# Optimization experiments

Measured on AMD Instinct MI355X. Metric: run time of the kernel, lower is better.

## Reference

```python
import jax, jax.numpy as jnp
import numpy as np

B, DIM, H, W = 8, 384, 64, 64
HEADS, KD, RATIO = 8, 32, 2
D = RATIO * KD            # 64, per-head value dim
NH_KD = HEADS * KD        # 256
DH = HEADS * D            # 512
N = H * W


def conv1x1_bn(x, Wc, scale, bias):
    # 1x1 conv (no bias) + BatchNorm2d in eval mode folds to per-channel affine.
    y = jnp.einsum('bchw,oc->bohw', x, Wc)
    return y * scale[:, None, None] + bias[:, None, None]


def setup_inputs() -> dict:
    key = jax.random.key(0)
    ks = jax.random.split(key, 13)
    f32 = jnp.float32
    inp = {
        'x': jax.random.normal(ks[0], (B, DIM, H, W), f32),
        'Wq': jax.random.normal(ks[1], (NH_KD, DIM), f32) * (1.0 / np.sqrt(DIM)),
        'sq': jax.random.uniform(ks[2], (NH_KD,), f32, 0.5, 1.5),
        'bq': jax.random.normal(ks[3], (NH_KD,), f32) * 0.1,
        'Wk': jax.random.normal(ks[4], (NH_KD, DIM), f32) * (1.0 / np.sqrt(DIM)),
        'sk': jax.random.uniform(ks[5], (NH_KD,), f32, 0.5, 1.5),
        'bk': jax.random.normal(ks[6], (NH_KD,), f32) * 0.1,
        'Wv': jax.random.normal(ks[7], (DH, DIM), f32) * (1.0 / np.sqrt(DIM)),
        'sv': jax.random.uniform(ks[8], (DH,), f32, 0.5, 1.5),
        'bv': jax.random.normal(ks[9], (DH,), f32) * 0.1,
        'Wp': jax.random.normal(ks[10], (DIM, DH), f32) * (1.0 / np.sqrt(DH)),
        'sp': jax.random.uniform(ks[11], (DIM,), f32, 0.5, 1.5),
        'bp': jax.random.normal(ks[12], (DIM,), f32) * 0.1,
    }
    return inp


def reference(x, Wq, sq, bq, Wk, sk, bk, Wv, sv, bv, Wp, sp, bp):
    # Q/K/V projections (1x1 conv + BN), reshaped to per-head [B, h, c, N]
    q = conv1x1_bn(x, Wq, sq, bq).reshape(B, HEADS, KD, N)
    k = conv1x1_bn(x, Wk, sk, bk).reshape(B, HEADS, KD, N)
    v = conv1x1_bn(x, Wv, sv, bv).reshape(B, HEADS, D, N)
    # dual softmax: keys over spatial dim, queries over channel dim
    key_sm = jax.nn.softmax(k, axis=3)
    query_sm = jax.nn.softmax(q, axis=2)
    # context = key @ value^T : [B,h,kd,d]
    context = jnp.einsum('bhkn,bhdn->bhkd', key_sm, v)
    # attended = context^T @ query : [B,h,d,N]
    attended = jnp.einsum('bhkd,bhkn->bhdn', context, query_sm)
    attended = attended.reshape(B, DH, H, W)
    # proj: activation (ReLU) then 1x1 conv + BN
    out = conv1x1_bn(jax.nn.relu(attended), Wp, sp, bp)
    return out
```

## Files before the change

kernel.cpp:

```cpp
#include <hip/hip_runtime.h>

typedef __attribute__((ext_vector_type(8))) short bf16x8;
typedef __attribute__((ext_vector_type(4))) float f32x4;
typedef __attribute__((ext_vector_type(4))) unsigned short us4;

__device__ __forceinline__ unsigned short f2bf(float f) {
    unsigned int u = __builtin_bit_cast(unsigned int, f);
    u = (u + 0x7FFFu + ((u >> 16) & 1u)) >> 16;
    return (unsigned short)u;
}
__device__ __forceinline__ float bf2f(unsigned short h) {
    return __builtin_bit_cast(float, (unsigned int)h << 16);
}

__global__ __launch_bounds__(256) void fold_weights_k(
    const float* __restrict__ Wq, const float* __restrict__ sq, const float* __restrict__ bq,
    const float* __restrict__ Wk, const float* __restrict__ sk, const float* __restrict__ bk,
    const float* __restrict__ Wv, const float* __restrict__ sv, const float* __restrict__ bv,
    const float* __restrict__ Wp, const float* __restrict__ sp,
    unsigned short* __restrict__ WqkvP, unsigned short* __restrict__ Wpf, float* __restrict__ bqkvP)
{
    int i = blockIdx.x * 256 + threadIdx.x;
    if (i < 393216) {
        int r = i / 384, c = i - r * 384;
        int head = r >> 7, t = r & 127;
        float w, s;
        if (t < 32)      { int ch = head * 32 + t;        w = Wq[ch * 384 + c]; s = sq[ch]; }
        else if (t < 64) { int ch = head * 32 + (t - 32); w = Wk[ch * 384 + c]; s = sk[ch]; }
        else             { int ch = head * 64 + (t - 64); w = Wv[ch * 384 + c]; s = sv[ch]; }
        WqkvP[i] = f2bf(w * s);
    } else if (i < 589824) {
        int j = i - 393216;
        Wpf[j] = f2bf(Wp[j] * sp[j >> 9]);
    } else if (i < 590848) {
        int r = i - 589824;
        int head = r >> 7, t = r & 127;
        bqkvP[r] = (t < 32) ? bq[head * 32 + t]
                 : (t < 64) ? bk[head * 32 + (t - 32)]
                            : bv[head * 64 + (t - 64)];
    }
}

__global__ __launch_bounds__(256, 3) void gemm_qkv_k(
    const unsigned short* __restrict__ A,
    const float* __restrict__ x,
    const float* __restrict__ bias,
    unsigned short* __restrict__ q_out,
    float* __restrict__ part,
    float* __restrict__ psums)
{
    __shared__ unsigned short As[3 * 4096];
    __shared__ unsigned short Bs[3 * 4096];
    const int tid = threadIdx.x;
    const int lane = tid & 63;
    const int w = tid >> 6, wr = w >> 1, wc = w & 1;
    const int li = lane & 15, g = lane >> 4;
    const int b = blockIdx.z, head = blockIdx.y, chunk = blockIdx.x;
    const int n0 = chunk * 128, m0 = head * 128;
    const float* xb = x + (long)b * 384 * 4096 + n0 + 2 * lane;

    const int i0 = tid, i1 = tid + 256;
    const int p0 = i0 >> 3, v0 = (i0 & 7) ^ (p0 & 7);
    const int p1 = i1 >> 3, v1 = (i1 & 7) ^ (p1 & 7);
    const long aro0 = (long)m0 * 384 + (long)(p0 * 2 + (v0 >> 2)) * 384 + (v0 & 3) * 8;
    const long aro1 = (long)m0 * 384 + (long)(p1 * 2 + (v1 >> 2)) * 384 + (v1 & 3) * 8;

#define ISSUE_A(kt) { const int _bf = (kt) % 3; const int _k0 = (kt) * 32; \
    __builtin_amdgcn_global_load_lds( \
        (const __attribute__((address_space(1))) void*)(A + aro0 + _k0), \
        (__attribute__((address_space(3))) void*)(As + _bf * 4096 + (size_t)i0 * 8), 16, 0, 0); \
    __builtin_amdgcn_global_load_lds( \
        (const __attribute__((address_space(1))) void*)(A + aro1 + _k0), \
        (__attribute__((address_space(3))) void*)(As + _bf * 4096 + (size_t)i1 * 8), 16, 0, 0); }

#define ISSUE_B(kt, breg) { const int _k0 = (kt) * 32 + w * 8; \
    _Pragma("unroll") \
    for (int j = 0; j < 8; ++j) \
        breg[j] = *reinterpret_cast<const float2*>(xb + (long)(_k0 + j) * 4096); }

#define WRITE_B(breg, _bf) { \
    unsigned int pw0[4], pw1[4]; \
    _Pragma("unroll") \
    for (int j = 0; j < 4; ++j) { \
        asm("v_cvt_pk_bf16_f32 %0, %1, %2" : "=v"(pw0[j]) : "v"(breg[2*j].x), "v"(breg[2*j+1].x)); \
        asm("v_cvt_pk_bf16_f32 %0, %1, %2" : "=v"(pw1[j]) : "v"(breg[2*j].y), "v"(breg[2*j+1].y)); \
    } \
    uint4 q0 = {pw0[0], pw0[1], pw0[2], pw0[3]}; \
    uint4 q1 = {pw1[0], pw1[1], pw1[2], pw1[3]}; \
    int s0 = w ^ (lane & 7), s1 = (4 + w) ^ (lane & 7); \
    *reinterpret_cast<uint4*>(Bs + (_bf) * 4096 + lane * 64 + s0 * 8) = q0; \
    *reinterpret_cast<uint4*>(Bs + (_bf) * 4096 + lane * 64 + s1 * 8) = q1; }

    float2 bregA[8], bregB[8];
    ISSUE_A(0); ISSUE_B(0, bregA);
    ISSUE_A(1); ISSUE_B(1, bregB);
    WRITE_B(bregA, 0);
    asm volatile("s_waitcnt vmcnt(10) lgkmcnt(0)\n\ts_barrier" ::: "memory");
    __builtin_amdgcn_sched_barrier(0);

    f32x4 acc[4][4];
    #pragma unroll
    for (int i = 0; i < 4; ++i)
        #pragma unroll
        for (int j = 0; j < 4; ++j) acc[i][j] = (f32x4){0.f, 0.f, 0.f, 0.f};

    #pragma unroll
    for (int kt = 0; kt < 12; ++kt) {
        const unsigned short* Ab = As + (kt % 3) * 4096;
        const unsigned short* Bl = Bs + (kt % 3) * 4096;

        bf16x8 av[4], bv[4];
        #pragma unroll
        for (int mf = 0; mf < 4; ++mf) {
            int r = wr * 64 + mf * 16 + li;
            int p = r >> 1;
            int slot = (((r & 1) * 4 + g) ^ (p & 7));
            av[mf] = *reinterpret_cast<const bf16x8*>(Ab + p * 64 + slot * 8);
        }
        #pragma unroll
        for (int nf = 0; nf < 4; ++nf) {
            int r = wc * 64 + nf * 16 + li;
            int p = r >> 1;
            int slot = (((r & 1) * 4 + g) ^ (p & 7));
            bv[nf] = *reinterpret_cast<const bf16x8*>(Bl + p * 64 + slot * 8);
        }
        if (kt < 10) {
            ISSUE_A(kt + 2);
            if (kt & 1) { ISSUE_B(kt + 2, bregB) }
            else        { ISSUE_B(kt + 2, bregA) }
        }
        __builtin_amdgcn_s_setprio(1);
        #pragma unroll
        for (int mf = 0; mf < 4; ++mf)
            #pragma unroll
            for (int nf = 0; nf < 4; ++nf)
                acc[mf][nf] = __builtin_amdgcn_mfma_f32_16x16x32_bf16(av[mf], bv[nf], acc[mf][nf], 0, 0, 0);
        __builtin_amdgcn_s_setprio(0);
        if (kt < 11) {
            if (kt & 1) { WRITE_B(bregA, (kt + 1) % 3) }
            else        { WRITE_B(bregB, (kt + 1) % 3) }
            asm volatile("s_waitcnt lgkmcnt(0)\n\ts_barrier" ::: "memory");
            __builtin_amdgcn_sched_barrier(0);
        }
    }
#undef ISSUE_A
#undef ISSUE_B
#undef WRITE_B

    __syncthreads();

    unsigned short* Ksh = As;
    unsigned short* Vsh = As + 4096;
    float* psl = reinterpret_cast<float*>(Bs);

    if (wr == 0) {
        #pragma unroll
        for (int mf = 0; mf < 2; ++mf) {
            int ml = mf * 16 + g * 4;
            #pragma unroll
            for (int nf = 0; nf < 4; ++nf) {
                int n = n0 + wc * 64 + nf * 16 + li;
                f32x4 v = acc[mf][nf];
                us4 o = { f2bf(v.x + bias[m0 + ml]),     f2bf(v.y + bias[m0 + ml + 1]),
                          f2bf(v.z + bias[m0 + ml + 2]), f2bf(v.w + bias[m0 + ml + 3]) };
                *reinterpret_cast<us4*>(q_out + (((long)b * 4096 + n) << 8) + head * 32 + ml) = o;
            }
        }
        float rs[2][4] = {{0.f,0.f,0.f,0.f},{0.f,0.f,0.f,0.f}};
        #pragma unroll
        for (int mm = 0; mm < 2; ++mm) {
            #pragma unroll
            for (int nf = 0; nf < 4; ++nf) {
                int nl = wc * 64 + nf * 16 + li;
                f32x4 v = acc[mm + 2][nf];
                #pragma unroll
                for (int r = 0; r < 4; ++r) {
                    int kd = mm * 16 + g * 4 + r;
                    float e = __expf(v[r] + bias[m0 + 32 + kd]);
                    rs[mm][r] += e;
                    Ksh[kd * 128 + ((((nl >> 3) ^ (kd & 7)) << 3) | (nl & 7))] = f2bf(e);
                }
            }
        }
        #pragma unroll
        for (int mm = 0; mm < 2; ++mm)
            #pragma unroll
            for (int r = 0; r < 4; ++r) {
                float s = rs[mm][r];
                s += __shfl_xor(s, 1); s += __shfl_xor(s, 2);
                s += __shfl_xor(s, 4); s += __shfl_xor(s, 8);
                if (li == 0) psl[wc * 32 + mm * 16 + g * 4 + r] = s;
            }
    } else {
        #pragma unroll
        for (int mf = 0; mf < 4; ++mf) {
            #pragma unroll
            for (int nf = 0; nf < 4; ++nf) {
                int nl = wc * 64 + nf * 16 + li;
                f32x4 v = acc[mf][nf];
                #pragma unroll
                for (int r = 0; r < 4; ++r) {
                    int d = mf * 16 + g * 4 + r;
                    Vsh[d * 128 + ((((nl >> 3) ^ (d & 7)) << 3) | (nl & 7))] =
                        f2bf(v[r] + bias[m0 + 64 + d]);
                }
            }
        }
    }
    __syncthreads();

    f32x4 c2[2] = {(f32x4){0.f,0.f,0.f,0.f}, (f32x4){0.f,0.f,0.f,0.f}};
    #pragma unroll
    for (int ks = 0; ks < 4; ++ks) {
        int rd = w * 16 + li;
        bf16x8 a0 = *reinterpret_cast<const bf16x8*>(Ksh + li * 128        + ((((ks * 4 + g) ^ (li & 7)) << 3)));
        bf16x8 a1 = *reinterpret_cast<const bf16x8*>(Ksh + (16 + li) * 128 + ((((ks * 4 + g) ^ ((16 + li) & 7)) << 3)));
        bf16x8 bb = *reinterpret_cast<const bf16x8*>(Vsh + rd * 128        + ((((ks * 4 + g) ^ (rd & 7)) << 3)));
        c2[0] = __builtin_amdgcn_mfma_f32_16x16x32_bf16(a0, bb, c2[0], 0, 0, 0);
        c2[1] = __builtin_amdgcn_mfma_f32_16x16x32_bf16(a1, bb, c2[1], 0, 0, 0);
    }
    const int bh = b * 8 + head;
    const long pbase = ((long)chunk * 64 + bh) * 2048;
    #pragma unroll
    for (int mm = 0; mm < 2; ++mm)
        *reinterpret_cast<f32x4*>(&part[pbase + (long)(w * 16 + li) * 32 + mm * 16 + g * 4]) = c2[mm];
    if (tid < 32)
        psums[((long)chunk * 64 + bh) * 32 + tid] = psl[tid] + psl[32 + tid];
}

__global__ __launch_bounds__(256) void ctx_reduce_k(const float* __restrict__ part,
                                                    const float* __restrict__ psums,
                                                    unsigned short* __restrict__ ctxT)
{
    int t = blockIdx.x * 256 + threadIdx.x;
    int bh = t >> 11, i = t & 2047;
    int kd = i & 31;
    float s = 0.f, den = 0.f;
    #pragma unroll
    for (int c = 0; c < 32; ++c) {
        s   += part[((long)c * 64 + bh) * 2048 + i];
        den += psums[((long)c * 64 + bh) * 32 + kd];
    }
    ctxT[t] = f2bf(s / den);
}

__global__ __launch_bounds__(512, 2) void proj_fused_k(
    const unsigned short* __restrict__ Wpf,
    const unsigned short* __restrict__ qT,
    const unsigned short* __restrict__ ctxT,
    const float* __restrict__ bp,
    float* __restrict__ out)
{
    __shared__ unsigned short Bsh[128 * 64];
    __shared__ unsigned short As[2][384 * 64];
    const int tid = threadIdx.x, lane = tid & 63, w = tid >> 6;
    const int li = lane & 15, g = lane >> 4;
    const int b = blockIdx.y, n0 = blockIdx.x * 128;

#define PROJ_STAGE(buf, s) { \
    _Pragma("unroll") \
    for (int j = 0; j < 6; ++j) { \
        int idx = j * 512 + tid; \
        int r = idx >> 3; \
        int ls = ((idx & 7) ^ (r & 7)) * 8; \
        __builtin_amdgcn_global_load_lds( \
            (const __attribute__((address_space(1))) void*)(Wpf + (long)r * 512 + (s) * 64 + ls), \
            (__attribute__((address_space(3))) void*)(As[buf] + (size_t)idx * 8), 16, 0, 0); \
    } }

    PROJ_STAGE(0, 0);

    f32x4 acc[3][8];
    #pragma unroll
    for (int i = 0; i < 3; ++i)
        #pragma unroll
        for (int j = 0; j < 8; ++j) acc[i][j] = (f32x4){0.f, 0.f, 0.f, 0.f};

    for (int s = 0; s < 8; ++s) {
        const unsigned short* cb = ctxT + ((long)b * 8 + s) * 2048;
        bf16x8 ca[4], pb;
        #pragma unroll
        for (int df = 0; df < 4; ++df)
            ca[df] = *reinterpret_cast<const bf16x8*>(cb + (df * 16 + li) * 32 + g * 8);
        {
            int n = n0 + w * 16 + li;
            bf16x8 r = *reinterpret_cast<const bf16x8*>(
                qT + (((long)b * 4096 + n) << 8) + s * 32 + g * 8);
            float f[8];
            float mx = -1e30f;
            #pragma unroll
            for (int j = 0; j < 8; ++j) { f[j] = bf2f((unsigned short)r[j]); mx = fmaxf(mx, f[j]); }
            mx = fmaxf(mx, __shfl_xor(mx, 16));
            mx = fmaxf(mx, __shfl_xor(mx, 32));
            float sm = 0.f;
            #pragma unroll
            for (int j = 0; j < 8; ++j) { f[j] = __expf(f[j] - mx); sm += f[j]; }
            sm += __shfl_xor(sm, 16);
            sm += __shfl_xor(sm, 32);
            float inv = 1.f / sm;
            #pragma unroll
            for (int j = 0; j < 8; ++j) pb[j] = (short)f2bf(f[j] * inv);
        }
        us4 bw[4];
        #pragma unroll
        for (int df = 0; df < 4; ++df) {
            f32x4 d = (f32x4){0.f, 0.f, 0.f, 0.f};
            d = __builtin_amdgcn_mfma_f32_16x16x32_bf16(ca[df], pb, d, 0, 0, 0);
            bw[df] = (us4){ f2bf(fmaxf(d.x, 0.f)), f2bf(fmaxf(d.y, 0.f)),
                            f2bf(fmaxf(d.z, 0.f)), f2bf(fmaxf(d.w, 0.f)) };
        }

        __syncthreads();

        if (s < 7) PROJ_STAGE((s + 1) & 1, s + 1);

        #pragma unroll
        for (int df = 0; df < 4; ++df) {
            int n = w * 16 + li;
            int slot = (df * 2 + (g >> 1)) ^ (n & 7);
            *reinterpret_cast<us4*>(Bsh + n * 64 + slot * 8 + (g & 1) * 4) = bw[df];
        }

        asm volatile("s_waitcnt lgkmcnt(0)\n\ts_barrier" ::: "memory");
        __builtin_amdgcn_sched_barrier(0);

        const unsigned short* Ab = As[s & 1];
        #pragma unroll
        for (int kk = 0; kk < 2; ++kk) {
            bf16x8 av[3], bv[8];
            #pragma unroll
            for (int mf = 0; mf < 3; ++mf) {
                int row = w * 48 + mf * 16 + li;
                int ps = ((kk * 4 + g) ^ (row & 7)) * 8;
                av[mf] = *reinterpret_cast<const bf16x8*>(Ab + row * 64 + ps);
            }
            #pragma unroll
            for (int nf = 0; nf < 8; ++nf) {
                int nn = nf * 16 + li;
                int ps = ((kk * 4 + g) ^ (nn & 7)) * 8;
                bv[nf] = *reinterpret_cast<const bf16x8*>(Bsh + nn * 64 + ps);
            }
            #pragma unroll
            for (int mf = 0; mf < 3; ++mf)
                #pragma unroll
                for (int nf = 0; nf < 8; ++nf)
                    acc[mf][nf] = __builtin_amdgcn_mfma_f32_16x16x32_bf16(av[mf], bv[nf], acc[mf][nf], 0, 0, 0);
        }
    }
#undef PROJ_STAGE

    #pragma unroll
    for (int mf = 0; mf < 3; ++mf) {
        int m = w * 48 + mf * 16 + g * 4;
        #pragma unroll
        for (int nf = 0; nf < 8; ++nf) {
            int n = n0 + nf * 16 + li;
            f32x4 v = acc[mf][nf];
            #pragma unroll
            for (int r = 0; r < 4; ++r)
                out[((long)b * 384 + m + r) * 4096 + n] = v[r] + bp[m + r];
        }
    }
}

extern "C" void kernel_launch(void* const* d_in, const int* in_sizes, int n_in,
                              void* d_out, int out_size, void* d_ws, size_t ws_size,
                              hipStream_t stream) {
    (void)in_sizes; (void)n_in; (void)out_size; (void)ws_size;
    const float* x  = (const float*)d_in[0];
    const float* Wq = (const float*)d_in[1];
    const float* sq = (const float*)d_in[2];
    const float* bq = (const float*)d_in[3];
    const float* Wk = (const float*)d_in[4];
    const float* sk = (const float*)d_in[5];
    const float* bk = (const float*)d_in[6];
    const float* Wv = (const float*)d_in[7];
    const float* sv = (const float*)d_in[8];
    const float* bv = (const float*)d_in[9];
    const float* Wp = (const float*)d_in[10];
    const float* sp = (const float*)d_in[11];
    const float* bp = (const float*)d_in[12];
    float* out = (float*)d_out;

    char* wsb = (char*)d_ws;
    unsigned short* Wqkv  = (unsigned short*)(wsb);
    unsigned short* Wpf   = (unsigned short*)(wsb + 786432);
    float*          bqkv  = (float*)(wsb + 1179648);
    unsigned short* ctxT  = (unsigned short*)(wsb + 1183744);
    float*          part  = (float*)(wsb + 1445888);
    float*          psums = (float*)(wsb + 18223104);
    unsigned short* qT    = (unsigned short*)(wsb + 18485248);

    fold_weights_k<<<2308, 256, 0, stream>>>(Wq, sq, bq, Wk, sk, bk, Wv, sv, bv, Wp, sp,
                                             Wqkv, Wpf, bqkv);
    gemm_qkv_k<<<dim3(32, 8, 8), 256, 0, stream>>>(Wqkv, x, bqkv, qT, part, psums);
    ctx_reduce_k<<<512, 256, 0, stream>>>(part, psums, ctxT);
    proj_fused_k<<<dim3(32, 8), 512, 0, stream>>>(Wpf, qT, ctxT, bp, out);
}
```

Measured before the change: 89.90 us.

## Stage x tile once in LDS and loop over heads inside QKV GEMM block

The QKV projection kernel now keeps the whole 384x128 bf16 x tile for one spatial chunk resident in shared memory and loops over head pairs inside the block (two wave-groups of four, one head each), instead of launching a separate block per head that re-reads and re-converts x. This removes the eightfold redundant global reads and fp32-to-bf16 conversion of x, while only the weight tiles are streamed through a triple buffer. In exchange the grid shrinks from 2048 to 256 blocks of 512 threads with much larger LDS use, which lowers occupancy and parallelism and serialises the head loop within a block.

```diff
diff --git a/kernel.cpp b/kernel.cpp
--- a/kernel.cpp
+++ b/kernel.cpp
@@ -41,7 +41,7 @@
     }
 }
 
-__global__ __launch_bounds__(256, 3) void gemm_qkv_k(
+__global__ __launch_bounds__(512, 2) void gemm_qkv_k(
     const unsigned short* __restrict__ A,
     const float* __restrict__ x,
     const float* __restrict__ bias,
@@ -49,36 +49,36 @@
     float* __restrict__ part,
     float* __restrict__ psums)
 {
-    __shared__ unsigned short As[3 * 4096];
-    __shared__ unsigned short Bs[3 * 4096];
+    __shared__ unsigned short Bp[12 * 4096];
+    __shared__ unsigned short As[3 * 8192];
+    __shared__ float psl2[2][64];
     const int tid = threadIdx.x;
     const int lane = tid & 63;
-    const int w = tid >> 6, wr = w >> 1, wc = w & 1;
+    const int w = tid >> 6;
+    const int hw = w & 3, hg = w >> 2;
+    const int wr = hw >> 1, wc = hw & 1;
     const int li = lane & 15, g = lane >> 4;
-    const int b = blockIdx.z, head = blockIdx.y, chunk = blockIdx.x;
-    const int n0 = chunk * 128, m0 = head * 128;
+    const int b = blockIdx.y, chunk = blockIdx.x;
+    const int n0 = chunk * 128;
     const float* xb = x + (long)b * 384 * 4096 + n0 + 2 * lane;
 
-    const int i0 = tid, i1 = tid + 256;
-    const int p0 = i0 >> 3, v0 = (i0 & 7) ^ (p0 & 7);
-    const int p1 = i1 >> 3, v1 = (i1 & 7) ^ (p1 & 7);
-    const long aro0 = (long)m0 * 384 + (long)(p0 * 2 + (v0 >> 2)) * 384 + (v0 & 3) * 8;
-    const long aro1 = (long)m0 * 384 + (long)(p1 * 2 + (v1 >> 2)) * 384 + (v1 & 3) * 8;
-
-#define ISSUE_A(kt) { const int _bf = (kt) % 3; const int _k0 = (kt) * 32; \
+    const int pA = tid >> 3, vA = (tid & 7) ^ (pA & 7);
+    const long aoff = (long)(pA * 2 + (vA >> 2)) * 384 + (vA & 3) * 8;
+
+#define ISSUE_A(hp, t) { const int _bf = (t) % 3; const long _k0 = (t) * 32; \
+    const unsigned short* _a0 = A + (long)(2 * (hp)) * 128 * 384 + aoff + _k0; \
     __builtin_amdgcn_global_load_lds( \
-        (const __attribute__((address_space(1))) void*)(A + aro0 + _k0), \
-        (__attribute__((address_space(3))) void*)(As + _bf * 4096 + (size_t)i0 * 8), 16, 0, 0); \
+        (const __attribute__((address_space(1))) void*)_a0, \
+        (__attribute__((address_space(3))) void*)(As + _bf * 8192 + (size_t)tid * 8), 16, 0, 0); \
     __builtin_amdgcn_global_load_lds( \
-        (const __attribute__((address_space(1))) void*)(A + aro1 + _k0), \
-        (__attribute__((address_space(3))) void*)(As + _bf * 4096 + (size_t)i1 * 8), 16, 0, 0); }
-
-#define ISSUE_B(kt, breg) { const int _k0 = (kt) * 32 + w * 8; \
+        (const __attribute__((address_space(1))) void*)(_a0 + 128 * 384), \
+        (__attribute__((address_space(3))) void*)(As + _bf * 8192 + 4096 + (size_t)tid * 8), 16, 0, 0); }
+
+#define LOADX(ktb, breg) { const int _k0 = ((ktb) + hg) * 32 + hw * 8; \
     _Pragma("unroll") \
     for (int j = 0; j < 8; ++j) \
         breg[j] = *reinterpret_cast<const float2*>(xb + (long)(_k0 + j) * 4096); }
-
-#define WRITE_B(breg, _bf) { \
+#define PACKX(ktb, breg) { \
     unsigned int pw0[4], pw1[4]; \
     _Pragma("unroll") \
     for (int j = 0; j < 4; ++j) { \
@@ -87,145 +87,157 @@
     } \
     uint4 q0 = {pw0[0], pw0[1], pw0[2], pw0[3]}; \
     uint4 q1 = {pw1[0], pw1[1], pw1[2], pw1[3]}; \
-    int s0 = w ^ (lane & 7), s1 = (4 + w) ^ (lane & 7); \
-    *reinterpret_cast<uint4*>(Bs + (_bf) * 4096 + lane * 64 + s0 * 8) = q0; \
-    *reinterpret_cast<uint4*>(Bs + (_bf) * 4096 + lane * 64 + s1 * 8) = q1; }
-
-    float2 bregA[8], bregB[8];
-    ISSUE_A(0); ISSUE_B(0, bregA);
-    ISSUE_A(1); ISSUE_B(1, bregB);
-    WRITE_B(bregA, 0);
-    asm volatile("s_waitcnt vmcnt(10) lgkmcnt(0)\n\ts_barrier" ::: "memory");
+    int s0 = hw ^ (lane & 7), s1 = (4 + hw) ^ (lane & 7); \
+    unsigned short* _bd = Bp + ((ktb) + hg) * 4096 + lane * 64; \
+    *reinterpret_cast<uint4*>(_bd + s0 * 8) = q0; \
+    *reinterpret_cast<uint4*>(_bd + s1 * 8) = q1; }
+
+    {
+        float2 ba[8], bb[8];
+        LOADX(0, ba);
+        #pragma unroll
+        for (int ktb = 0; ktb < 12; ktb += 2) {
+            if (ktb < 10) { if ((ktb >> 1) & 1) { LOADX(ktb + 2, ba) } else { LOADX(ktb + 2, bb) } }
+            if ((ktb >> 1) & 1) { PACKX(ktb, bb) } else { PACKX(ktb, ba) }
+        }
+    }
+#undef LOADX
+#undef PACKX
+
+    ISSUE_A(0, 0); ISSUE_A(0, 1);
+    asm volatile("s_waitcnt lgkmcnt(0)\n\ts_barrier" ::: "memory");
     __builtin_amdgcn_sched_barrier(0);
 
-    f32x4 acc[4][4];
-    #pragma unroll
-    for (int i = 0; i < 4; ++i)
-        #pragma unroll
-        for (int j = 0; j < 4; ++j) acc[i][j] = (f32x4){0.f, 0.f, 0.f, 0.f};
-
-    #pragma unroll
-    for (int kt = 0; kt < 12; ++kt) {
-        const unsigned short* Ab = As + (kt % 3) * 4096;
-        const unsigned short* Bl = Bs + (kt % 3) * 4096;
-
-        bf16x8 av[4], bv[4];
-        #pragma unroll
-        for (int mf = 0; mf < 4; ++mf) {
-            int r = wr * 64 + mf * 16 + li;
-            int p = r >> 1;
-            int slot = (((r & 1) * 4 + g) ^ (p & 7));
-            av[mf] = *reinterpret_cast<const bf16x8*>(Ab + p * 64 + slot * 8);
-        }
-        #pragma unroll
-        for (int nf = 0; nf < 4; ++nf) {
-            int r = wc * 64 + nf * 16 + li;
-            int p = r >> 1;
-            int slot = (((r & 1) * 4 + g) ^ (p & 7));
-            bv[nf] = *reinterpret_cast<const bf16x8*>(Bl + p * 64 + slot * 8);
-        }
-        if (kt < 10) {
-            ISSUE_A(kt + 2);
-            if (kt & 1) { ISSUE_B(kt + 2, bregB) }
-            else        { ISSUE_B(kt + 2, bregA) }
-        }
-        __builtin_amdgcn_s_setprio(1);
-        #pragma unroll
-        for (int mf = 0; mf < 4; ++mf)
-            #pragma unroll
-            for (int nf = 0; nf < 4; ++nf)
-                acc[mf][nf] = __builtin_amdgcn_mfma_f32_16x16x32_bf16(av[mf], bv[nf], acc[mf][nf], 0, 0, 0);
-        __builtin_amdgcn_s_setprio(0);
-        if (kt < 11) {
-            if (kt & 1) { WRITE_B(bregA, (kt + 1) % 3) }
-            else        { WRITE_B(bregB, (kt + 1) % 3) }
-            asm volatile("s_waitcnt lgkmcnt(0)\n\ts_barrier" ::: "memory");
+    for (int hp = 0; hp < 4; ++hp) {
+        const int head = 2 * hp + hg;
+        const int m0 = head * 128;
+
+        f32x4 acc[4][4];
+        #pragma unroll
+        for (int i = 0; i < 4; ++i)
+            #pragma unroll
+            for (int j = 0; j < 4; ++j) acc[i][j] = (f32x4){0.f, 0.f, 0.f, 0.f};
+
+        #pragma unroll
+        for (int kt = 0; kt < 12; ++kt) {
+            if (kt < 11) asm volatile("s_waitcnt vmcnt(2)\n\ts_barrier" ::: "memory");
+            else         asm volatile("s_waitcnt vmcnt(0)\n\ts_barrier" ::: "memory");
             __builtin_amdgcn_sched_barrier(0);
-        }
+
+            const unsigned short* Ab = As + (kt % 3) * 8192 + hg * 4096;
+            const unsigned short* Bl = Bp + kt * 4096;
+
+            bf16x8 av[4], bv[4];
+            #pragma unroll
+            for (int mf = 0; mf < 4; ++mf) {
+                int r = wr * 64 + mf * 16 + li;
+                int p = r >> 1;
+                int slot = (((r & 1) * 4 + g) ^ (p & 7));
+                av[mf] = *reinterpret_cast<const bf16x8*>(Ab + p * 64 + slot * 8);
+            }
+            #pragma unroll
+            for (int nf = 0; nf < 4; ++nf) {
+                int r = wc * 64 + nf * 16 + li;
+                int p = r >> 1;
+                int slot = (((r & 1) * 4 + g) ^ (p & 7));
+                bv[nf] = *reinterpret_cast<const bf16x8*>(Bl + p * 64 + slot * 8);
+            }
+            if (kt < 10)      ISSUE_A(hp, kt + 2);
+            __builtin_amdgcn_s_setprio(1);
+            #pragma unroll
+            for (int mf = 0; mf < 4; ++mf)
+                #pragma unroll
+                for (int nf = 0; nf < 4; ++nf)
+                    acc[mf][nf] = __builtin_amdgcn_mfma_f32_16x16x32_bf16(av[mf], bv[nf], acc[mf][nf], 0, 0, 0);
+            __builtin_amdgcn_s_setprio(0);
+        }
+
+        __syncthreads();
+
+        unsigned short* Ksh = As + hg * 12288;
+        unsigned short* Vsh = Ksh + 4096;
+        float* psl = psl2[hg];
+
+        if (wr == 0) {
+            #pragma unroll
+            for (int mf = 0; mf < 2; ++mf) {
+                int ml = mf * 16 + g * 4;
+                #pragma unroll
+                for (int nf = 0; nf < 4; ++nf) {
+                    int n = n0 + wc * 64 + nf * 16 + li;
+                    f32x4 v = acc[mf][nf];
+                    us4 o = { f2bf(v.x + bias[m0 + ml]),     f2bf(v.y + bias[m0 + ml + 1]),
+                              f2bf(v.z + bias[m0 + ml + 2]), f2bf(v.w + bias[m0 + ml + 3]) };
+                    *reinterpret_cast<us4*>(q_out + (((long)b * 4096 + n) << 8) + head * 32 + ml) = o;
+                }
+            }
+            float rs[2][4] = {{0.f,0.f,0.f,0.f},{0.f,0.f,0.f,0.f}};
+            #pragma unroll
+            for (int mm = 0; mm < 2; ++mm) {
+                #pragma unroll
+                for (int nf = 0; nf < 4; ++nf) {
+                    int nl = wc * 64 + nf * 16 + li;
+                    f32x4 v = acc[mm + 2][nf];
+                    #pragma unroll
+                    for (int r = 0; r < 4; ++r) {
+                        int kd = mm * 16 + g * 4 + r;
+                        float e = __expf(v[r] + bias[m0 + 32 + kd]);
+                        rs[mm][r] += e;
+                        Ksh[kd * 128 + ((((nl >> 3) ^ (kd & 7)) << 3) | (nl & 7))] = f2bf(e);
+                    }
+                }
+            }
+            #pragma unroll
+            for (int mm = 0; mm < 2; ++mm)
+                #pragma unroll
+                for (int r = 0; r < 4; ++r) {
+                    float s = rs[mm][r];
+                    s += __shfl_xor(s, 1); s += __shfl_xor(s, 2);
+                    s += __shfl_xor(s, 4); s += __shfl_xor(s, 8);
+                    if (li == 0) psl[wc * 32 + mm * 16 + g * 4 + r] = s;
+                }
+        } else {
+            #pragma unroll
+            for (int mf = 0; mf < 4; ++mf) {
+                #pragma unroll
+                for (int nf = 0; nf < 4; ++nf) {
+                    int nl = wc * 64 + nf * 16 + li;
+                    f32x4 v = acc[mf][nf];
+                    #pragma unroll
+                    for (int r = 0; r < 4; ++r) {
+                        int d = mf * 16 + g * 4 + r;
+                        Vsh[d * 128 + ((((nl >> 3) ^ (d & 7)) << 3) | (nl & 7))] =
+                            f2bf(v[r] + bias[m0 + 64 + d]);
+                    }
+                }
+            }
+        }
+        __syncthreads();
+
+        f32x4 c2[2] = {(f32x4){0.f,0.f,0.f,0.f}, (f32x4){0.f,0.f,0.f,0.f}};
+        #pragma unroll
+        for (int ks = 0; ks < 4; ++ks) {
+            int rd = hw * 16 + li;
+            bf16x8 a0 = *reinterpret_cast<const bf16x8*>(Ksh + li * 128        + ((((ks * 4 + g) ^ (li & 7)) << 3)));
+            bf16x8 a1 = *reinterpret_cast<const bf16x8*>(Ksh + (16 + li) * 128 + ((((ks * 4 + g) ^ ((16 + li) & 7)) << 3)));
+            bf16x8 bb = *reinterpret_cast<const bf16x8*>(Vsh + rd * 128        + ((((ks * 4 + g) ^ (rd & 7)) << 3)));
+            c2[0] = __builtin_amdgcn_mfma_f32_16x16x32_bf16(a0, bb, c2[0], 0, 0, 0);
+            c2[1] = __builtin_amdgcn_mfma_f32_16x16x32_bf16(a1, bb, c2[1], 0, 0, 0);
+        }
+        const int bh = b * 8 + head;
+        const long pbase = ((long)chunk * 64 + bh) * 2048;
+        #pragma unroll
+        for (int mm = 0; mm < 2; ++mm)
+            *reinterpret_cast<f32x4*>(&part[pbase + (long)(hw * 16 + li) * 32 + mm * 16 + g * 4]) = c2[mm];
+        if (tid < 64)
+            psums[((long)chunk * 64 + b * 8 + 2 * hp + (tid >> 5)) * 32 + (tid & 31)] =
+                psl2[tid >> 5][tid & 31] + psl2[tid >> 5][32 + (tid & 31)];
+
+        __syncthreads();
+
+        if (hp < 3) { ISSUE_A(hp + 1, 0); ISSUE_A(hp + 1, 1); }
     }
 #undef ISSUE_A
-#undef ISSUE_B
-#undef WRITE_B
-
-    __syncthreads();
-
-    unsigned short* Ksh = As;
-    unsigned short* Vsh = As + 4096;
-    float* psl = reinterpret_cast<float*>(Bs);
-
-    if (wr == 0) {
-        #pragma unroll
-        for (int mf = 0; mf < 2; ++mf) {
-            int ml = mf * 16 + g * 4;
-            #pragma unroll
-            for (int nf = 0; nf < 4; ++nf) {
-                int n = n0 + wc * 64 + nf * 16 + li;
-                f32x4 v = acc[mf][nf];
-                us4 o = { f2bf(v.x + bias[m0 + ml]),     f2bf(v.y + bias[m0 + ml + 1]),
-                          f2bf(v.z + bias[m0 + ml + 2]), f2bf(v.w + bias[m0 + ml + 3]) };
-                *reinterpret_cast<us4*>(q_out + (((long)b * 4096 + n) << 8) + head * 32 + ml) = o;
-            }
-        }
-        float rs[2][4] = {{0.f,0.f,0.f,0.f},{0.f,0.f,0.f,0.f}};
-        #pragma unroll
-        for (int mm = 0; mm < 2; ++mm) {
-            #pragma unroll
-            for (int nf = 0; nf < 4; ++nf) {
-                int nl = wc * 64 + nf * 16 + li;
-                f32x4 v = acc[mm + 2][nf];
-                #pragma unroll
-                for (int r = 0; r < 4; ++r) {
-                    int kd = mm * 16 + g * 4 + r;
-                    float e = __expf(v[r] + bias[m0 + 32 + kd]);
-                    rs[mm][r] += e;
-                    Ksh[kd * 128 + ((((nl >> 3) ^ (kd & 7)) << 3) | (nl & 7))] = f2bf(e);
-                }
-            }
-        }
-        #pragma unroll
-        for (int mm = 0; mm < 2; ++mm)
-            #pragma unroll
-            for (int r = 0; r < 4; ++r) {
-                float s = rs[mm][r];
-                s += __shfl_xor(s, 1); s += __shfl_xor(s, 2);
-                s += __shfl_xor(s, 4); s += __shfl_xor(s, 8);
-                if (li == 0) psl[wc * 32 + mm * 16 + g * 4 + r] = s;
-            }
-    } else {
-        #pragma unroll
-        for (int mf = 0; mf < 4; ++mf) {
-            #pragma unroll
-            for (int nf = 0; nf < 4; ++nf) {
-                int nl = wc * 64 + nf * 16 + li;
-                f32x4 v = acc[mf][nf];
-                #pragma unroll
-                for (int r = 0; r < 4; ++r) {
-                    int d = mf * 16 + g * 4 + r;
-                    Vsh[d * 128 + ((((nl >> 3) ^ (d & 7)) << 3) | (nl & 7))] =
-                        f2bf(v[r] + bias[m0 + 64 + d]);
-                }
-            }
-        }
-    }
-    __syncthreads();
-
-    f32x4 c2[2] = {(f32x4){0.f,0.f,0.f,0.f}, (f32x4){0.f,0.f,0.f,0.f}};
-    #pragma unroll
-    for (int ks = 0; ks < 4; ++ks) {
-        int rd = w * 16 + li;
-        bf16x8 a0 = *reinterpret_cast<const bf16x8*>(Ksh + li * 128        + ((((ks * 4 + g) ^ (li & 7)) << 3)));
-        bf16x8 a1 = *reinterpret_cast<const bf16x8*>(Ksh + (16 + li) * 128 + ((((ks * 4 + g) ^ ((16 + li) & 7)) << 3)));
-        bf16x8 bb = *reinterpret_cast<const bf16x8*>(Vsh + rd * 128        + ((((ks * 4 + g) ^ (rd & 7)) << 3)));
-        c2[0] = __builtin_amdgcn_mfma_f32_16x16x32_bf16(a0, bb, c2[0], 0, 0, 0);
-        c2[1] = __builtin_amdgcn_mfma_f32_16x16x32_bf16(a1, bb, c2[1], 0, 0, 0);
-    }
-    const int bh = b * 8 + head;
-    const long pbase = ((long)chunk * 64 + bh) * 2048;
-    #pragma unroll
-    for (int mm = 0; mm < 2; ++mm)
-        *reinterpret_cast<f32x4*>(&part[pbase + (long)(w * 16 + li) * 32 + mm * 16 + g * 4]) = c2[mm];
-    if (tid < 32)
-        psums[((long)chunk * 64 + bh) * 32 + tid] = psl[tid] + psl[32 + tid];
 }
 
 __global__ __launch_bounds__(256) void ctx_reduce_k(const float* __restrict__ part,
@@ -393,7 +405,7 @@
 
     fold_weights_k<<<2308, 256, 0, stream>>>(Wq, sq, bq, Wk, sk, bk, Wv, sv, bv, Wp, sp,
                                              Wqkv, Wpf, bqkv);
-    gemm_qkv_k<<<dim3(32, 8, 8), 256, 0, stream>>>(Wqkv, x, bqkv, qT, part, psums);
+    gemm_qkv_k<<<dim3(32, 8), 512, 0, stream>>>(Wqkv, x, bqkv, qT, part, psums);
     ctx_reduce_k<<<512, 256, 0, stream>>>(part, psums, ctxT);
     proj_fused_k<<<dim3(32, 8), 512, 0, stream>>>(Wpf, qT, ctxT, bp, out);
 }
```

After: 88.07 us. 1.02x faster.
